# Kernel optimization log

Hardware: AMD Instinct MI355X
Metric: run time of the kernel (lower is better)

The kernel has to match this reference:

```python
import jax, jax.numpy as jnp
import numpy as np
from jax import lax

STRIDES = (8, 16, 32, 64, 128)
LEVEL_HW = ((100, 128), (50, 64), (25, 32), (13, 16), (7, 8))
NUM_CLASSES = 80
PRE_NMS_THRESH = 0.05
PRE_NMS_TOPK = 1000
NMS_THRESH = 0.6
MAX_DET = 100
CLS_OFFSET = 1.0e4  # > max image coordinate, separates classes for joint NMS


def setup_inputs() -> dict:
    key = jax.random.key(0)
    B = 16
    ks = jax.random.split(key, 3 * len(LEVEL_HW))
    inp = {}
    i = 0
    for lvl, (h, w) in enumerate(LEVEL_HW):
        # shift logits down so sigmoid scores are mostly below the 0.05 candidate
        # threshold (realistic detection sparsity)
        inp[f"logits_p{lvl + 3}"] = jax.random.normal(ks[i], (B, NUM_CLASSES, h, w), jnp.float32) - 4.0; i += 1
        inp[f"bbox_p{lvl + 3}"] = jax.random.uniform(ks[i], (B, 4, h, w), jnp.float32, minval=0.0, maxval=64.0); i += 1
        inp[f"ctr_p{lvl + 3}"] = jax.random.normal(ks[i], (B, 1, h, w), jnp.float32); i += 1
    inp["im_info"] = jnp.tile(jnp.array([[800.0, 1024.0]], jnp.float32), (B, 1))
    return inp


def _locations(h, w, stride):
    # FCOSLocation: center of each stride cell -> [HW, 2] as (x, y)
    sx = jnp.arange(w, dtype=jnp.float32) * stride + stride // 2
    sy = jnp.arange(h, dtype=jnp.float32) * stride + stride // 2
    yy, xx = jnp.meshgrid(sy, sx, indexing="ij")
    return jnp.stack([xx.reshape(-1), yy.reshape(-1)], axis=-1)


def _nms_single(boxes, scores, classes):
    # boxes [K,4], scores [K] (descending), classes [K] int
    off = classes.astype(jnp.float32)[:, None] * CLS_OFFSET
    nb = boxes + off  # class-offset trick -> per-class NMS in one pass
    areas = jnp.maximum(nb[:, 2] - nb[:, 0], 0.0) * jnp.maximum(nb[:, 3] - nb[:, 1], 0.0)

    def body(sc, _):
        i = jnp.argmax(sc)
        s = sc[i]
        bi = nb[i]
        xx1 = jnp.maximum(bi[0], nb[:, 0])
        yy1 = jnp.maximum(bi[1], nb[:, 1])
        xx2 = jnp.minimum(bi[2], nb[:, 2])
        yy2 = jnp.minimum(bi[3], nb[:, 3])
        inter = jnp.maximum(xx2 - xx1, 0.0) * jnp.maximum(yy2 - yy1, 0.0)
        iou = inter / (areas[i] + areas - inter + 1e-9)
        sc2 = jnp.where(iou >= NMS_THRESH, -jnp.inf, sc).at[i].set(-jnp.inf)
        return sc2, (i, s > 0.0)

    _, (idxs, valid) = lax.scan(body, scores, None, length=MAX_DET)
    det = jnp.concatenate(
        [boxes[idxs], scores[idxs][:, None], classes[idxs].astype(jnp.float32)[:, None]],
        axis=-1,
    )  # [MAX_DET, 6] = x1,y1,x2,y2,score,class
    return jnp.where(valid[:, None], det, 0.0)


def _forward(logits_p3, bbox_p3, ctr_p3, logits_p4, bbox_p4, ctr_p4,
             logits_p5, bbox_p5, ctr_p5, logits_p6, bbox_p6, ctr_p6,
             logits_p7, bbox_p7, ctr_p7, im_info):
    levels = [(logits_p3, bbox_p3, ctr_p3), (logits_p4, bbox_p4, ctr_p4),
              (logits_p5, bbox_p5, ctr_p5), (logits_p6, bbox_p6, ctr_p6),
              (logits_p7, bbox_p7, ctr_p7)]
    scores_l, boxes_l = [], []
    for (lg, rg, ct), stride in zip(levels, STRIDES):
        B, C, H, W = lg.shape
        cls = jax.nn.sigmoid(lg).transpose(0, 2, 3, 1).reshape(B, H * W, C)
        cen = jax.nn.sigmoid(ct).transpose(0, 2, 3, 1).reshape(B, H * W, 1)
        # candidate threshold on raw class prob, then modulate by centerness
        comb = jnp.where(cls > PRE_NMS_THRESH, cls * cen, 0.0)
        locs = _locations(H, W, stride)  # [HW, 2]
        reg = rg.transpose(0, 2, 3, 1).reshape(B, H * W, 4)  # (l, t, r, b)
        bx = jnp.stack([locs[None, :, 0] - reg[..., 0],
                        locs[None, :, 1] - reg[..., 1],
                        locs[None, :, 0] + reg[..., 2],
                        locs[None, :, 1] + reg[..., 3]], axis=-1)
        scores_l.append(comb)
        boxes_l.append(bx)
    scores = jnp.concatenate(scores_l, axis=1)  # [B, N, C]
    boxes = jnp.concatenate(boxes_l, axis=1)    # [B, N, 4]
    B, N, C = scores.shape
    vals, idx = lax.top_k(scores.reshape(B, N * C), PRE_NMS_TOPK)  # [B, K]
    loc = idx // C
    cls_id = idx % C
    cand = jnp.take_along_axis(boxes, loc[..., None], axis=1)  # [B, K, 4]
    h = im_info[:, 0:1]
    w = im_info[:, 1:2]
    x1 = jnp.clip(cand[..., 0], 0.0, w - 1.0)
    y1 = jnp.clip(cand[..., 1], 0.0, h - 1.0)
    x2 = jnp.clip(cand[..., 2], 0.0, w - 1.0)
    y2 = jnp.clip(cand[..., 3], 0.0, h - 1.0)
    cand = jnp.stack([x1, y1, x2, y2], axis=-1)
    sc = jnp.where(vals > 0.0, jnp.sqrt(jnp.maximum(vals, 0.0) + 1e-12), 0.0)
    return jax.vmap(_nms_single)(cand, sc, cls_id)  # [B, MAX_DET, 6]


def reference(logits_p3, bbox_p3, ctr_p3, logits_p4, bbox_p4, ctr_p4,
              logits_p5, bbox_p5, ctr_p5, logits_p6, bbox_p6, ctr_p6,
              logits_p7, bbox_p7, ctr_p7, im_info):
    return _forward(logits_p3, bbox_p3, ctr_p3, logits_p4, bbox_p4, ctr_p4,
                    logits_p5, bbox_p5, ctr_p5, logits_p6, bbox_p6, ctr_p6,
                    logits_p7, bbox_p7, ctr_p7, im_info)
```

## Files before the change

kernel.cpp:

```cpp
#include <hip/hip_runtime.h>
#include <math.h>

#pragma clang fp contract(off)

#define NB 16
#define NC 80
#define NTOT 17064
#define TOPK 1000
#define NBINS 8192
#define CAP 4096
#define MAXDET 100
#define NREP 4
#define CNTSTRIDE 64

struct Ptrs {
    const float* lg[5];
    const float* bb[5];
    const float* ct[5];
};

__device__ __forceinline__ void level_of(int n, int& l, int& hw, int& W,
                                         int& stride, int& half, int& HW) {
    if (n < 12800)      { l = 0; hw = n;         W = 128; stride = 8;   half = 4;  HW = 12800; }
    else if (n < 16000) { l = 1; hw = n - 12800; W = 64;  stride = 16;  half = 8;  HW = 3200;  }
    else if (n < 16800) { l = 2; hw = n - 16000; W = 32;  stride = 32;  half = 16; HW = 800;   }
    else if (n < 17008) { l = 3; hw = n - 16800; W = 16;  stride = 64;  half = 32; HW = 208;   }
    else                { l = 4; hw = n - 17008; W = 8;   stride = 128; half = 64; HW = 56;    }
}

template<int HW4, int NF4>
__device__ __forceinline__ void hist_level(const float* lgb, const float* ctb,
                                           int tid, int bx, int gx, unsigned* lh) {
    for (int i0 = bx * 256; i0 < NF4; i0 += gx * 256) {
        int i = i0 + tid;
        if (i < NF4) {
            int c   = i / HW4;
            int hwf = i - c * HW4;
            float4 v  = *(const float4*)(lgb + c * (HW4 * 4) + hwf * 4);
            if (v.x > -2.95f || v.y > -2.95f || v.z > -2.95f || v.w > -2.95f) {
                float4 cv = *(const float4*)(ctb + hwf * 4);
                float xs[4] = {v.x, v.y, v.z, v.w};
                float cs[4] = {cv.x, cv.y, cv.z, cv.w};
#pragma unroll
                for (int j = 0; j < 4; ++j) {
                    float x = xs[j];
                    if (x > -2.95f) {
                        float cls = 1.0f / (1.0f + expf(-x));
                        if (cls > 0.05f) {
                            float cen = 1.0f / (1.0f + expf(-cs[j]));
                            float comb = cls * cen;
                            atomicAdd(&lh[__float_as_uint(comb) >> 19], 1u);
                        }
                    }
                }
            }
        }
    }
}

__global__ void __launch_bounds__(256) k_histA(Ptrs p, unsigned* hist) {
    __shared__ unsigned lh[NBINS];
    int b = blockIdx.y, tid = threadIdx.x, bx = blockIdx.x, gx = gridDim.x;
    for (int i = tid; i < NBINS; i += 256) lh[i] = 0;
    __syncthreads();

    hist_level<3200, 256000>(p.lg[0] + (size_t)b * NC * 12800, p.ct[0] + (size_t)b * 12800, tid, bx, gx, lh);
    hist_level< 800,  64000>(p.lg[1] + (size_t)b * NC * 3200,  p.ct[1] + (size_t)b * 3200,  tid, bx, gx, lh);
    hist_level< 200,  16000>(p.lg[2] + (size_t)b * NC * 800,   p.ct[2] + (size_t)b * 800,   tid, bx, gx, lh);
    hist_level<  52,   4160>(p.lg[3] + (size_t)b * NC * 208,   p.ct[3] + (size_t)b * 208,   tid, bx, gx, lh);
    hist_level<  14,   1120>(p.lg[4] + (size_t)b * NC * 56,    p.ct[4] + (size_t)b * 56,    tid, bx, gx, lh);

    __syncthreads();
    unsigned* h = hist + ((size_t)(bx & (NREP - 1)) * NB + b) * NBINS;
    for (int i = tid; i < NBINS; i += 256) {
        unsigned v = lh[i];
        if (v) atomicAdd(&h[i], v);
    }
}

__global__ void __launch_bounds__(256) k_thresh(const unsigned* hist, unsigned* T) {
    __shared__ unsigned hl[NBINS];
    __shared__ unsigned wtot[4];
    __shared__ int Tf;
    int b = blockIdx.x, tid = threadIdx.x, lane = tid & 63, wv = tid >> 6;
    if (tid == 0) Tf = 0;
    for (int i = tid; i < NBINS; i += 256) {
        unsigned s = 0;
        for (int r = 0; r < NREP; ++r)
            s += hist[((size_t)r * NB + b) * NBINS + i];
        hl[i] = s;
    }
    __syncthreads();
    int base = tid * 32;
    unsigned mysum = 0;
#pragma unroll
    for (int i = 0; i < 32; ++i) mysum += hl[base + i];
    unsigned incl = mysum;
#pragma unroll
    for (int off = 1; off < 64; off <<= 1) {
        unsigned v = __shfl_down(incl, off);
        if (lane + off < 64) incl += v;
    }
    if (lane == 0) wtot[wv] = incl;
    __syncthreads();
    unsigned above = 0;
    for (int w = wv + 1; w < 4; ++w) above += wtot[w];
    unsigned sufincl = incl + above;
    unsigned excl = sufincl - mysum;
    if (excl < TOPK && sufincl >= TOPK) {
        unsigned running = excl;
        for (int bin = base + 31; bin >= base; --bin) {
            running += hl[bin];
            if (running >= TOPK) { Tf = bin; break; }
        }
    }
    __syncthreads();
    if (tid == 0) T[b] = (unsigned)Tf;
}

template<int HW4, int NF4, int LVOFF>
__device__ __forceinline__ void compact_level(const float* lgb, const float* ctb,
        int tid, int lane, int bx, int gx, unsigned Tb, float xpre,
        unsigned* cntb, unsigned long long* selb, unsigned long long ltmask) {
    for (int i0 = bx * 256; i0 < NF4; i0 += gx * 256) {
        int i = i0 + tid;
        bool f0 = false, f1 = false, f2 = false, f3 = false;
        unsigned long long k0 = 0, k1 = 0, k2 = 0, k3 = 0;
        if (i < NF4) {
            int c   = i / HW4;
            int hwf = i - c * HW4;
            float4 v = *(const float4*)(lgb + c * (HW4 * 4) + hwf * 4);
            if (v.x > xpre || v.y > xpre || v.z > xpre || v.w > xpre) {
                float4 cv = *(const float4*)(ctb + hwf * 4);
                int nbase = LVOFF + hwf * 4;
#define DO_J(J, X, CT, F, K)                                                  \
                if ((X) > xpre) {                                             \
                    float cls = 1.0f / (1.0f + expf(-(X)));                   \
                    if (cls > 0.05f) {                                        \
                        float cen = 1.0f / (1.0f + expf(-(CT)));              \
                        float comb = cls * cen;                               \
                        unsigned bits = __float_as_uint(comb);                \
                        if ((bits >> 19) >= Tb) {                             \
                            unsigned idx = (unsigned)((nbase + (J)) * NC + c);\
                            K = ((unsigned long long)bits << 32) |            \
                                (0xFFFFFFFFu - idx);                          \
                            F = true;                                         \
                        }                                                     \
                    }                                                         \
                }
                DO_J(0, v.x, cv.x, f0, k0)
                DO_J(1, v.y, cv.y, f1, k1)
                DO_J(2, v.z, cv.z, f2, k2)
                DO_J(3, v.w, cv.w, f3, k3)
#undef DO_J
            }
        }
        unsigned long long m0 = __ballot(f0), m1 = __ballot(f1);
        unsigned long long m2 = __ballot(f2), m3 = __ballot(f3);
        if ((m0 | m1 | m2 | m3) == 0ULL) continue;
        unsigned t0 = (unsigned)__popcll(m0), t1 = (unsigned)__popcll(m1);
        unsigned t2 = (unsigned)__popcll(m2), t3 = (unsigned)__popcll(m3);
        unsigned total = t0 + t1 + t2 + t3;
        int basep = 0;
        if (lane == 0) basep = (int)atomicAdd(cntb, total);
        basep = __shfl(basep, 0);
        if (f0) { int pos = basep + (int)__popcll(m0 & ltmask);                       if (pos < CAP) selb[pos] = k0; }
        if (f1) { int pos = basep + (int)t0 + (int)__popcll(m1 & ltmask);             if (pos < CAP) selb[pos] = k1; }
        if (f2) { int pos = basep + (int)(t0 + t1) + (int)__popcll(m2 & ltmask);      if (pos < CAP) selb[pos] = k2; }
        if (f3) { int pos = basep + (int)(t0 + t1 + t2) + (int)__popcll(m3 & ltmask); if (pos < CAP) selb[pos] = k3; }
    }
}

__global__ void __launch_bounds__(256) k_compactB(Ptrs p, const unsigned* T,
                                                  unsigned* cnt2, unsigned long long* sel) {
    int b = blockIdx.y, tid = threadIdx.x, lane = tid & 63;
    int bx = blockIdx.x, gx = gridDim.x;
    unsigned Tb = T[b];
    float mthr = __uint_as_float(Tb << 19);
    float xpre = -2.95f;
    if (mthr > 1e-37f && mthr < 1.0f) {
        float lm = logf(mthr / (1.0f - mthr)) - 0.01f;
        if (lm > xpre) xpre = lm;
    }
    unsigned long long ltmask = (1ULL << lane) - 1ULL;
    unsigned* cntb = cnt2 + (size_t)b * CNTSTRIDE;
    unsigned long long* selb = sel + (size_t)b * CAP;
    compact_level<3200, 256000,     0>(p.lg[0] + (size_t)b * NC * 12800, p.ct[0] + (size_t)b * 12800, tid, lane, bx, gx, Tb, xpre, cntb, selb, ltmask);
    compact_level< 800,  64000, 12800>(p.lg[1] + (size_t)b * NC * 3200,  p.ct[1] + (size_t)b * 3200,  tid, lane, bx, gx, Tb, xpre, cntb, selb, ltmask);
    compact_level< 200,  16000, 16000>(p.lg[2] + (size_t)b * NC * 800,   p.ct[2] + (size_t)b * 800,   tid, lane, bx, gx, Tb, xpre, cntb, selb, ltmask);
    compact_level<  52,   4160, 16800>(p.lg[3] + (size_t)b * NC * 208,   p.ct[3] + (size_t)b * 208,   tid, lane, bx, gx, Tb, xpre, cntb, selb, ltmask);
    compact_level<  14,   1120, 17008>(p.lg[4] + (size_t)b * NC * 56,    p.ct[4] + (size_t)b * 56,    tid, lane, bx, gx, Tb, xpre, cntb, selb, ltmask);
}

__global__ void __launch_bounds__(1024) k_selnms(Ptrs p, const unsigned* cnt,
                                                 const unsigned long long* sel,
                                                 const float* im_info, float* out) {
    __shared__ __align__(16) unsigned long long keys[CAP + 2];
    __shared__ float4 nbx[TOPK];
    __shared__ float  sarea[TOPK];
    __shared__ float4 obox[TOPK];
    __shared__ float2 oscl[TOPK];
    int b = blockIdx.x, tid = threadIdx.x, lane = tid & 63;

    unsigned M = cnt[(size_t)b * CNTSTRIDE];
    if (M > CAP) M = CAP;
    int Mpad = (int)((M + 1u) & ~1u);
    for (int i = tid; i < Mpad; i += 1024)
        keys[i] = (i < (int)M) ? sel[(size_t)b * CAP + i] : 0ULL;
    __syncthreads();

    float Him = im_info[b * 2 + 0], Wim = im_info[b * 2 + 1];
    float xmax = Wim - 1.0f, ymax = Him - 1.0f;

    for (int i = tid; i < (int)M; i += 1024) {
        unsigned long long k = keys[i];
        int rank = 0;
        for (int j = 0; j < Mpad; j += 2) {
            ulonglong2 kk = *(const ulonglong2*)&keys[j];
            rank += (kk.x > k) ? 1 : 0;
            rank += (kk.y > k) ? 1 : 0;
        }
        if (rank < TOPK) {
            unsigned sb = (unsigned)(k >> 32);
            unsigned idx = 0xFFFFFFFFu - (unsigned)(k & 0xFFFFFFFFu);
            float val = __uint_as_float(sb);
            int n = idx / NC, c = idx - n * NC;
            int l, hw, W, stride, half, HW;
            level_of(n, l, hw, W, stride, half, HW);
            int wx = hw % W, hy = hw / W;
            float locx = (float)(wx * stride + half);
            float locy = (float)(hy * stride + half);
            const float* bb = p.bb[l] + (size_t)b * 4 * HW + hw;
            float r0 = bb[0], r1 = bb[(size_t)HW], r2 = bb[(size_t)2 * HW], r3 = bb[(size_t)3 * HW];
            float x1 = locx - r0, y1 = locy - r1, x2 = locx + r2, y2 = locy + r3;
            x1 = fminf(fmaxf(x1, 0.f), xmax);
            y1 = fminf(fmaxf(y1, 0.f), ymax);
            x2 = fminf(fmaxf(x2, 0.f), xmax);
            y2 = fminf(fmaxf(y2, 0.f), ymax);
            float s = sqrtf(val + 1e-12f);
            float off = (float)c * 10000.0f;
            float a0 = x1 + off, a1 = y1 + off, a2 = x2 + off, a3 = y2 + off;
            nbx[rank] = make_float4(a0, a1, a2, a3);
            sarea[rank] = fmaxf(a2 - a0, 0.f) * fmaxf(a3 - a1, 0.f);
            obox[rank] = make_float4(x1, y1, x2, y2);
            oscl[rank] = make_float2(s, (float)c);
        }
    }
    __syncthreads();
    if (tid >= 64) return;

    int ncand = (int)M < TOPK ? (int)M : TOPK;
    int na = 0;
    float4 a0b = make_float4(0.f, 0.f, 0.f, 0.f);
    float4 a1b = make_float4(0.f, 0.f, 0.f, 0.f);
    float a0a = 0.f, a1a = 0.f;
    float* ob = out + (size_t)b * MAXDET * 6;

    for (int r = 0; r < ncand && na < MAXDET; ++r) {
        float4 cb = nbx[r];
        float ca = sarea[r];
        bool sup = false;
        if (lane < na) {
            float xx1 = fmaxf(a0b.x, cb.x);
            float yy1 = fmaxf(a0b.y, cb.y);
            float xx2 = fminf(a0b.z, cb.z);
            float yy2 = fminf(a0b.w, cb.w);
            float inter = fmaxf(xx2 - xx1, 0.f) * fmaxf(yy2 - yy1, 0.f);
            float iou = inter / (((a0a + ca) - inter) + 1e-9f);
            sup = (iou >= 0.6f);
        }
        if (lane + 64 < na) {
            float xx1 = fmaxf(a1b.x, cb.x);
            float yy1 = fmaxf(a1b.y, cb.y);
            float xx2 = fminf(a1b.z, cb.z);
            float yy2 = fminf(a1b.w, cb.w);
            float inter = fmaxf(xx2 - xx1, 0.f) * fmaxf(yy2 - yy1, 0.f);
            float iou = inter / (((a1a + ca) - inter) + 1e-9f);
            sup |= (iou >= 0.6f);
        }
        if (__ballot(sup) == 0ULL) {
            if (lane == (na & 63)) {
                if (na < 64) { a0b = cb; a0a = ca; }
                else         { a1b = cb; a1a = ca; }
            }
            if (lane == 0) {
                float4 o4 = obox[r]; float2 s2 = oscl[r];
                ob[na * 6 + 0] = o4.x; ob[na * 6 + 1] = o4.y;
                ob[na * 6 + 2] = o4.z; ob[na * 6 + 3] = o4.w;
                ob[na * 6 + 4] = s2.x; ob[na * 6 + 5] = s2.y;
            }
            ++na;
        }
    }
    for (int q = na * 6 + lane; q < MAXDET * 6; q += 64)
        ob[q] = 0.f;
}

extern "C" void kernel_launch(void* const* d_in, const int* in_sizes, int n_in,
                              void* d_out, int out_size, void* d_ws, size_t ws_size,
                              hipStream_t stream) {
    Ptrs p;
    for (int l = 0; l < 5; ++l) {
        p.lg[l] = (const float*)d_in[3 * l + 0];
        p.bb[l] = (const float*)d_in[3 * l + 1];
        p.ct[l] = (const float*)d_in[3 * l + 2];
    }
    const float* im_info = (const float*)d_in[15];
    float* out = (float*)d_out;

    unsigned char* w = (unsigned char*)d_ws;
    unsigned* hist          = (unsigned*)(w);
    unsigned* cnt2          = (unsigned*)(w + 2097152);
    unsigned* T             = (unsigned*)(w + 2101248);
    unsigned long long* sel = (unsigned long long*)(w + 2101504);

    hipMemsetAsync(w, 0, 2101504, stream);

    k_histA<<<dim3(64, NB), 256, 0, stream>>>(p, hist);
    k_thresh<<<NB, 256, 0, stream>>>(hist, T);
    k_compactB<<<dim3(128, NB), 256, 0, stream>>>(p, T, cnt2, sel);
    k_selnms<<<NB, 1024, 0, stream>>>(p, cnt2, sel, im_info, out);
}
```

Before: 264.4 us.

## Split rank/decode and NMS into separate kernels with wider rank parallelism

The combined select+NMS kernel (one 1024-thread block per image) is split in two. A rank/decode kernel spreads the O(M^2) rank counting over a 16xB grid of 256-thread blocks and writes the decoded top-K candidates to a workspace buffer. A single-wavefront NMS kernel then streams those candidates through shared memory in chunks. Histogram replication NREP drops from 4 to 2, shrinking the memset. The cost is an extra launch and a global round trip for the candidates, and each rank block reloads all keys.

After: 255.0 us. -3.6%, faster.

```diff
diff --git a/kernel.cpp b/kernel.cpp
--- a/kernel.cpp
+++ b/kernel.cpp
@@ -10,8 +10,9 @@
 #define NBINS 8192
 #define CAP 4096
 #define MAXDET 100
-#define NREP 4
+#define NREP 2
 #define CNTSTRIDE 64
+#define CHUNK 128
 
 struct Ptrs {
     const float* lg[5];
@@ -192,105 +193,120 @@
     compact_level<  14,   1120, 17008>(p.lg[4] + (size_t)b * NC * 56,    p.ct[4] + (size_t)b * 56,    tid, lane, bx, gx, Tb, xpre, cntb, selb, ltmask);
 }
 
-__global__ void __launch_bounds__(1024) k_selnms(Ptrs p, const unsigned* cnt,
+__global__ void __launch_bounds__(256) k_rankdec(Ptrs p, const unsigned* cnt,
                                                  const unsigned long long* sel,
-                                                 const float* im_info, float* out) {
-    __shared__ __align__(16) unsigned long long keys[CAP + 2];
-    __shared__ float4 nbx[TOPK];
-    __shared__ float  sarea[TOPK];
-    __shared__ float4 obox[TOPK];
-    __shared__ float2 oscl[TOPK];
-    int b = blockIdx.x, tid = threadIdx.x, lane = tid & 63;
-
+                                                 const float* im_info, float* cand) {
+    __shared__ __align__(16) unsigned long long keys[CAP];
+    int b = blockIdx.y, tid = threadIdx.x;
     unsigned M = cnt[(size_t)b * CNTSTRIDE];
     if (M > CAP) M = CAP;
+    int s0 = blockIdx.x * 256;
+    if (s0 >= (int)M) return;
     int Mpad = (int)((M + 1u) & ~1u);
-    for (int i = tid; i < Mpad; i += 1024)
+    for (int i = tid; i < Mpad; i += 256)
         keys[i] = (i < (int)M) ? sel[(size_t)b * CAP + i] : 0ULL;
     __syncthreads();
+
+    int s = s0 + tid;
+    if (s >= (int)M) return;
+    unsigned long long k = keys[s];
+    int rank = 0;
+    for (int j = 0; j < Mpad; j += 2) {
+        ulonglong2 kk = *(const ulonglong2*)&keys[j];
+        rank += (kk.x > k) ? 1 : 0;
+        rank += (kk.y > k) ? 1 : 0;
+    }
+    if (rank >= TOPK) return;
 
     float Him = im_info[b * 2 + 0], Wim = im_info[b * 2 + 1];
     float xmax = Wim - 1.0f, ymax = Him - 1.0f;
-
-    for (int i = tid; i < (int)M; i += 1024) {
-        unsigned long long k = keys[i];
-        int rank = 0;
-        for (int j = 0; j < Mpad; j += 2) {
-            ulonglong2 kk = *(const ulonglong2*)&keys[j];
-            rank += (kk.x > k) ? 1 : 0;
-            rank += (kk.y > k) ? 1 : 0;
-        }
-        if (rank < TOPK) {
-            unsigned sb = (unsigned)(k >> 32);
-            unsigned idx = 0xFFFFFFFFu - (unsigned)(k & 0xFFFFFFFFu);
-            float val = __uint_as_float(sb);
-            int n = idx / NC, c = idx - n * NC;
-            int l, hw, W, stride, half, HW;
-            level_of(n, l, hw, W, stride, half, HW);
-            int wx = hw % W, hy = hw / W;
-            float locx = (float)(wx * stride + half);
-            float locy = (float)(hy * stride + half);
-            const float* bb = p.bb[l] + (size_t)b * 4 * HW + hw;
-            float r0 = bb[0], r1 = bb[(size_t)HW], r2 = bb[(size_t)2 * HW], r3 = bb[(size_t)3 * HW];
-            float x1 = locx - r0, y1 = locy - r1, x2 = locx + r2, y2 = locy + r3;
-            x1 = fminf(fmaxf(x1, 0.f), xmax);
-            y1 = fminf(fmaxf(y1, 0.f), ymax);
-            x2 = fminf(fmaxf(x2, 0.f), xmax);
-            y2 = fminf(fmaxf(y2, 0.f), ymax);
-            float s = sqrtf(val + 1e-12f);
-            float off = (float)c * 10000.0f;
-            float a0 = x1 + off, a1 = y1 + off, a2 = x2 + off, a3 = y2 + off;
-            nbx[rank] = make_float4(a0, a1, a2, a3);
-            sarea[rank] = fmaxf(a2 - a0, 0.f) * fmaxf(a3 - a1, 0.f);
-            obox[rank] = make_float4(x1, y1, x2, y2);
-            oscl[rank] = make_float2(s, (float)c);
-        }
-    }
-    __syncthreads();
-    if (tid >= 64) return;
-
+    unsigned sb = (unsigned)(k >> 32);
+    unsigned idx = 0xFFFFFFFFu - (unsigned)(k & 0xFFFFFFFFu);
+    float val = __uint_as_float(sb);
+    int n = idx / NC, c = idx - n * NC;
+    int l, hw, W, stride, half, HW;
+    level_of(n, l, hw, W, stride, half, HW);
+    int wx = hw % W, hy = hw / W;
+    float locx = (float)(wx * stride + half);
+    float locy = (float)(hy * stride + half);
+    const float* bb = p.bb[l] + (size_t)b * 4 * HW + hw;
+    float r0 = bb[0], r1 = bb[(size_t)HW], r2 = bb[(size_t)2 * HW], r3 = bb[(size_t)3 * HW];
+    float x1 = locx - r0, y1 = locy - r1, x2 = locx + r2, y2 = locy + r3;
+    x1 = fminf(fmaxf(x1, 0.f), xmax);
+    y1 = fminf(fmaxf(y1, 0.f), ymax);
+    x2 = fminf(fmaxf(x2, 0.f), xmax);
+    y2 = fminf(fmaxf(y2, 0.f), ymax);
+    float scv = sqrtf(val + 1e-12f);
+    float off = (float)c * 10000.0f;
+    float a0 = x1 + off, a1 = y1 + off, a2 = x2 + off, a3 = y2 + off;
+    float area = fmaxf(a2 - a0, 0.f) * fmaxf(a3 - a1, 0.f);
+    float* dst = cand + ((size_t)b * TOPK + rank) * 12;
+    *(float4*)(dst + 0) = make_float4(x1, y1, x2, y2);
+    *(float4*)(dst + 4) = make_float4(a0, a1, a2, a3);
+    *(float4*)(dst + 8) = make_float4(area, scv, (float)c, 0.f);
+}
+
+__global__ void __launch_bounds__(64) k_nms(const unsigned* cnt, const float* cand,
+                                            float* out) {
+    __shared__ float4 s_ob[CHUNK], s_nb[CHUNK], s_ms[CHUNK];
+    int b = blockIdx.x, lane = threadIdx.x;
+    unsigned M = cnt[(size_t)b * CNTSTRIDE];
+    if (M > CAP) M = CAP;
     int ncand = (int)M < TOPK ? (int)M : TOPK;
+    const float* src = cand + (size_t)b * TOPK * 12;
+    float* ob = out + (size_t)b * MAXDET * 6;
+
     int na = 0;
     float4 a0b = make_float4(0.f, 0.f, 0.f, 0.f);
     float4 a1b = make_float4(0.f, 0.f, 0.f, 0.f);
     float a0a = 0.f, a1a = 0.f;
-    float* ob = out + (size_t)b * MAXDET * 6;
-
-    for (int r = 0; r < ncand && na < MAXDET; ++r) {
-        float4 cb = nbx[r];
-        float ca = sarea[r];
-        bool sup = false;
-        if (lane < na) {
-            float xx1 = fmaxf(a0b.x, cb.x);
-            float yy1 = fmaxf(a0b.y, cb.y);
-            float xx2 = fminf(a0b.z, cb.z);
-            float yy2 = fminf(a0b.w, cb.w);
-            float inter = fmaxf(xx2 - xx1, 0.f) * fmaxf(yy2 - yy1, 0.f);
-            float iou = inter / (((a0a + ca) - inter) + 1e-9f);
-            sup = (iou >= 0.6f);
-        }
-        if (lane + 64 < na) {
-            float xx1 = fmaxf(a1b.x, cb.x);
-            float yy1 = fmaxf(a1b.y, cb.y);
-            float xx2 = fminf(a1b.z, cb.z);
-            float yy2 = fminf(a1b.w, cb.w);
-            float inter = fmaxf(xx2 - xx1, 0.f) * fmaxf(yy2 - yy1, 0.f);
-            float iou = inter / (((a1a + ca) - inter) + 1e-9f);
-            sup |= (iou >= 0.6f);
-        }
-        if (__ballot(sup) == 0ULL) {
-            if (lane == (na & 63)) {
-                if (na < 64) { a0b = cb; a0a = ca; }
-                else         { a1b = cb; a1a = ca; }
-            }
-            if (lane == 0) {
-                float4 o4 = obox[r]; float2 s2 = oscl[r];
-                ob[na * 6 + 0] = o4.x; ob[na * 6 + 1] = o4.y;
-                ob[na * 6 + 2] = o4.z; ob[na * 6 + 3] = o4.w;
-                ob[na * 6 + 4] = s2.x; ob[na * 6 + 5] = s2.y;
-            }
-            ++na;
-        }
+
+    for (int base = 0; base < ncand && na < MAXDET; base += CHUNK) {
+        int cn = ncand - base; if (cn > CHUNK) cn = CHUNK;
+        for (int cidx = lane; cidx < cn; cidx += 64) {
+            const float* s = src + (size_t)(base + cidx) * 12;
+            s_ob[cidx] = *(const float4*)(s + 0);
+            s_nb[cidx] = *(const float4*)(s + 4);
+            s_ms[cidx] = *(const float4*)(s + 8);
+        }
+        __syncthreads();
+        for (int r = 0; r < cn && na < MAXDET; ++r) {
+            float4 cb = s_nb[r];
+            float ca = s_ms[r].x;
+            bool sup = false;
+            if (lane < na) {
+                float xx1 = fmaxf(a0b.x, cb.x);
+                float yy1 = fmaxf(a0b.y, cb.y);
+                float xx2 = fminf(a0b.z, cb.z);
+                float yy2 = fminf(a0b.w, cb.w);
+                float inter = fmaxf(xx2 - xx1, 0.f) * fmaxf(yy2 - yy1, 0.f);
+                float iou = inter / (((a0a + ca) - inter) + 1e-9f);
+                sup = (iou >= 0.6f);
+            }
+            if (lane + 64 < na) {
+                float xx1 = fmaxf(a1b.x, cb.x);
+                float yy1 = fmaxf(a1b.y, cb.y);
+                float xx2 = fminf(a1b.z, cb.z);
+                float yy2 = fminf(a1b.w, cb.w);
+                float inter = fmaxf(xx2 - xx1, 0.f) * fmaxf(yy2 - yy1, 0.f);
+                float iou = inter / (((a1a + ca) - inter) + 1e-9f);
+                sup |= (iou >= 0.6f);
+            }
+            if (__ballot(sup) == 0ULL) {
+                if (lane == (na & 63)) {
+                    if (na < 64) { a0b = cb; a0a = ca; }
+                    else         { a1b = cb; a1a = ca; }
+                }
+                if (lane == 0) {
+                    float4 o4 = s_ob[r]; float4 m4 = s_ms[r];
+                    ob[na * 6 + 0] = o4.x; ob[na * 6 + 1] = o4.y;
+                    ob[na * 6 + 2] = o4.z; ob[na * 6 + 3] = o4.w;
+                    ob[na * 6 + 4] = m4.y; ob[na * 6 + 5] = m4.z;
+                }
+                ++na;
+            }
+        }
+        __syncthreads();
     }
     for (int q = na * 6 + lane; q < MAXDET * 6; q += 64)
         ob[q] = 0.f;
@@ -310,14 +326,16 @@
 
     unsigned char* w = (unsigned char*)d_ws;
     unsigned* hist          = (unsigned*)(w);
-    unsigned* cnt2          = (unsigned*)(w + 2097152);
-    unsigned* T             = (unsigned*)(w + 2101248);
-    unsigned long long* sel = (unsigned long long*)(w + 2101504);
-
-    hipMemsetAsync(w, 0, 2101504, stream);
+    unsigned* cnt2          = (unsigned*)(w + 1048576);
+    unsigned* T             = (unsigned*)(w + 1052672);
+    unsigned long long* sel = (unsigned long long*)(w + 1052928);
+    float* cand             = (float*)(w + 1577216);
+
+    hipMemsetAsync(w, 0, 1052928, stream);
 
     k_histA<<<dim3(64, NB), 256, 0, stream>>>(p, hist);
     k_thresh<<<NB, 256, 0, stream>>>(hist, T);
     k_compactB<<<dim3(128, NB), 256, 0, stream>>>(p, T, cnt2, sel);
-    k_selnms<<<NB, 1024, 0, stream>>>(p, cnt2, sel, im_info, out);
-}
+    k_rankdec<<<dim3(16, NB), 256, 0, stream>>>(p, cnt2, sel, im_info, cand);
+    k_nms<<<NB, 64, 0, stream>>>(cnt2, cand, out);
+}
```
